# Kernel tuning notes

Measured on AMD Instinct MI355X. Metric: run time of the kernel, lower is better.

The kernel has to match this reference:

```python
import jax, jax.numpy as jnp
import numpy as np

NUM_TREES = 32
TREE_DEPTH = 6
INPUT_DIM = 256
SHRINKAGE = 0.1
PHI_NUMEL = 1
N_INTERNAL = (1 << TREE_DEPTH) - 1  # 63, heap-ordered (level by level)
N_LEAVES = 1 << TREE_DEPTH          # 64


def setup_inputs() -> dict:
    key = jax.random.key(0)
    kx, kw, kb, kp = jax.random.split(key, 4)
    x = jax.random.normal(kx, (16384, INPUT_DIM), dtype=jnp.float32)
    # All internal-node Linear(input_dim,1) weights, batched: [T, N, F], biases [T, N]
    lim = 1.0 / np.sqrt(INPUT_DIM)  # torch nn.Linear default uniform init scale
    W = jax.random.uniform(kw, (NUM_TREES, N_INTERNAL, INPUT_DIM), minval=-lim, maxval=lim, dtype=jnp.float32)
    b = jax.random.uniform(kb, (NUM_TREES, N_INTERNAL), minval=-lim, maxval=lim, dtype=jnp.float32)
    # Leaf values phi: [T, L, P] (original: randn per leaf)
    phi = jax.random.normal(kp, (NUM_TREES, N_LEAVES, PHI_NUMEL), dtype=jnp.float32)
    return {"x": x, "W": W, "b": b, "phi": phi}


def reference(x, W, b, phi):
    B = x.shape[0]
    T, N, F = W.shape
    # One batched GEMM for every internal node of every tree, then sigmoid.
    # probs[b, t, n] = sigmoid(x[b] . W[t, n] + b[t, n]); heap order: node n at
    # level d occupies slots [2^d - 1, 2^(d+1) - 2], children of slot i are 2i, 2i+1.
    probs = jax.nn.sigmoid(jnp.einsum('bf,tnf->btn', x, W) + b)  # [B, T, N]
    # Path probabilities down the tree: left child gets (1 - p), right gets p
    # (matches calculate_probabilities: left <- pp*(1-prob), right <- pp*prob).
    mu = jnp.ones((B, T, 1), dtype=probs.dtype)
    offset = 0
    depth = int(np.log2(N + 1))
    for d in range(depth):
        n = 1 << d
        p = probs[:, :, offset:offset + n]                      # [B, T, n]
        mu = jnp.stack([mu * (1.0 - p), mu * p], axis=-1)       # [B, T, n, 2]
        mu = mu.reshape(B, T, 2 * n)
        offset += n
    # mu: [B, T, L] leaf path probabilities. Per-tree pred = sum_l mu_l * phi_l;
    # GBM output = shrinkage * sum over trees.
    pred = SHRINKAGE * jnp.einsum('btl,tlp->bp', mu, phi)       # [B, P]
    return pred
```

## Files before the change

kernel.cpp:

```cpp
#include <hip/hip_runtime.h>
#include <cmath>

typedef unsigned short u16;
typedef __bf16 bf16x8 __attribute__((ext_vector_type(8)));
typedef float f32x4 __attribute__((ext_vector_type(4)));
typedef unsigned short u16x4 __attribute__((ext_vector_type(4)));

#define BATCH 16384
#define NTREE 32
#define NINT 63
#define NLEAF 64
#define FDIM 256
#define MT 128
#define BK 64
#define KSTEPS 4

typedef __attribute__((address_space(3))) void lvoid;
typedef __attribute__((address_space(1))) const void gvoid;
__device__ __forceinline__ void gload16(const void* g, void* l) {
    __builtin_amdgcn_global_load_lds((gvoid*)g, (lvoid*)l, 16, 0, 0);
}

__device__ __forceinline__ u16 f2bf(float f) {
    unsigned int x = __float_as_uint(f);
    x += 0x7fffu + ((x >> 16) & 1u);
    return (u16)(x >> 16);
}

__global__ void convert_kernel(const float* __restrict__ x, const float* __restrict__ W,
                               u16* __restrict__ xb, u16* __restrict__ Wb) {
    int idx = blockIdx.x * blockDim.x + threadIdx.x;
    int stride = gridDim.x * blockDim.x;
    const int NXQ = BATCH * FDIM / 4;
    for (int i = idx; i < NXQ; i += stride) {
        float4 v = ((const float4*)x)[i];
        u16x4 o = { f2bf(v.x), f2bf(v.y), f2bf(v.z), f2bf(v.w) };
        ((u16x4*)xb)[i] = o;
    }
    const int NWQ = NTREE * NLEAF * FDIM / 4;
    for (int i = idx; i < NWQ; i += stride) {
        int t = i / (NLEAF * FDIM / 4);
        int r = i % (NLEAF * FDIM / 4);
        int node = r / (FDIM / 4);
        int kq = r % (FDIM / 4);
        float4 v = make_float4(0.f, 0.f, 0.f, 0.f);
        if (node < NINT) v = ((const float4*)(W + ((size_t)t * NINT + node) * FDIM))[kq];
        u16x4 o = { f2bf(v.x), f2bf(v.y), f2bf(v.z), f2bf(v.w) };
        ((u16x4*)Wb)[i] = o;
    }
}

__global__ __launch_bounds__(256, 3) void softgbm_main(
    const u16* __restrict__ xb, const u16* __restrict__ Wb,
    const float* __restrict__ bg, const float* __restrict__ phig,
    float* __restrict__ partial) {
    union ShMem {
        struct { u16 A[2][MT * BK]; u16 B[2][NLEAF * BK]; } s;
        struct { float p[MT * 65]; float phi[NLEAF]; } e;
    };
    __shared__ ShMem sh;

    const int tid = threadIdx.x;
    const int lane = tid & 63, wv = tid >> 6;
    const int t = blockIdx.y;
    const int m0 = blockIdx.x * MT;

    const u16* agp[4]; const u16* bgp[2];
    #pragma unroll
    for (int j = 0; j < 4; ++j) {
        int cl = wv * 256 + j * 64 + lane;
        int row = cl >> 3, pcc = cl & 7;
        int cc = pcc ^ (row & 7);
        agp[j] = xb + (size_t)(m0 + row) * FDIM + cc * 8;
    }
    #pragma unroll
    for (int j = 0; j < 2; ++j) {
        int cl = wv * 128 + j * 64 + lane;
        int row = cl >> 3, pcc = cl & 7;
        int cc = pcc ^ (row & 7);
        bgp[j] = Wb + (size_t)(t * NLEAF + row) * FDIM + cc * 8;
    }

    const int wr = wv >> 1, wc = wv & 1;
    const int frow = lane & 15, lg = lane >> 4;
    int aoffs[4][2], boffs[2][2];
    #pragma unroll
    for (int ar = 0; ar < 4; ++ar) {
        int r = wr * 64 + ar * 16 + frow;
        #pragma unroll
        for (int ks = 0; ks < 2; ++ks) {
            int cc = ks * 4 + lg;
            aoffs[ar][ks] = r * 128 + ((cc ^ (r & 7)) * 16);
        }
    }
    #pragma unroll
    for (int bc = 0; bc < 2; ++bc) {
        int n = wc * 32 + bc * 16 + frow;
        #pragma unroll
        for (int ks = 0; ks < 2; ++ks) {
            int cc = ks * 4 + lg;
            boffs[bc][ks] = n * 128 + ((cc ^ (n & 7)) * 16);
        }
    }

    float bv[2];
    #pragma unroll
    for (int bc = 0; bc < 2; ++bc) {
        int col = wc * 32 + bc * 16 + frow;
        bv[bc] = (col < NINT) ? bg[t * NINT + col] : 0.f;
    }

    #pragma unroll
    for (int j = 0; j < 4; ++j)
        gload16(agp[j], &sh.s.A[0][(wv * 256 + j * 64) * 8]);
    #pragma unroll
    for (int j = 0; j < 2; ++j)
        gload16(bgp[j], &sh.s.B[0][(wv * 128 + j * 64) * 8]);
    __syncthreads();

    f32x4 acc[4][2] = {};
    #pragma unroll
    for (int st = 0; st < KSTEPS; ++st) {
        int cur = st & 1;
        if (st < KSTEPS - 1) {
            int nxt = cur ^ 1;
            #pragma unroll
            for (int j = 0; j < 4; ++j)
                gload16(agp[j] + (st + 1) * BK, &sh.s.A[nxt][(wv * 256 + j * 64) * 8]);
            #pragma unroll
            for (int j = 0; j < 2; ++j)
                gload16(bgp[j] + (st + 1) * BK, &sh.s.B[nxt][(wv * 128 + j * 64) * 8]);
        }
        const char* Ab = (const char*)sh.s.A[cur];
        const char* Bb = (const char*)sh.s.B[cur];
        #pragma unroll
        for (int ks = 0; ks < 2; ++ks) {
            bf16x8 af[4], bf_[2];
            #pragma unroll
            for (int ar = 0; ar < 4; ++ar) af[ar] = *(const bf16x8*)(Ab + aoffs[ar][ks]);
            #pragma unroll
            for (int bc = 0; bc < 2; ++bc) bf_[bc] = *(const bf16x8*)(Bb + boffs[bc][ks]);
            #pragma unroll
            for (int ar = 0; ar < 4; ++ar)
                #pragma unroll
                for (int bc = 0; bc < 2; ++bc)
                    acc[ar][bc] = __builtin_amdgcn_mfma_f32_16x16x32_bf16(af[ar], bf_[bc], acc[ar][bc], 0, 0, 0);
        }
        __syncthreads();
    }

    if (tid < NLEAF) sh.e.phi[tid] = phig[(size_t)t * NLEAF + tid];
    #pragma unroll
    for (int ar = 0; ar < 4; ++ar)
        #pragma unroll
        for (int bc = 0; bc < 2; ++bc)
            #pragma unroll
            for (int j = 0; j < 4; ++j) {
                int row = wr * 64 + ar * 16 + lg * 4 + j;
                int col = wc * 32 + bc * 16 + frow;
                float z = acc[ar][bc][j] + bv[bc];
                sh.e.p[row * 65 + col] = __builtin_amdgcn_rcpf(1.f + __expf(-z));
            }
    __syncthreads();

    {
        const int row = tid >> 1, hl = tid & 1;
        const float* pr = sh.e.p + row * 65;
        const float* pf = sh.e.phi + hl * 32;
        float p0 = pr[0];
        float mu[16];
        mu[0] = hl ? p0 : 1.f - p0;
        #pragma unroll
        for (int d = 1; d < 5; ++d) {
            int n = 1 << (d - 1);
            int off = (1 << d) - 1 + hl * n;
            #pragma unroll
            for (int i = n - 1; i >= 0; --i) {
                float p = pr[off + i];
                float m = mu[i];
                float tt = m * p;
                mu[2 * i + 1] = tt;
                mu[2 * i] = m - tt;
            }
        }
        float s = 0.f;
        #pragma unroll
        for (int i = 0; i < 16; ++i) {
            float p = pr[31 + hl * 16 + i];
            float a = pf[2 * i], b2 = pf[2 * i + 1];
            s += mu[i] * (a + p * (b2 - a));
        }
        s += __shfl_xor(s, 1);
        if (!hl) partial[(size_t)t * BATCH + m0 + row] = s;
    }
}

__global__ void reduce_kernel(const float* __restrict__ partial, float* __restrict__ out) {
    int i = blockIdx.x * 256 + threadIdx.x;
    float s = 0.f;
    #pragma unroll
    for (int t = 0; t < NTREE; ++t) s += partial[(size_t)t * BATCH + i];
    out[i] = 0.1f * s;
}

extern "C" void kernel_launch(void* const* d_in, const int* in_sizes, int n_in,
                              void* d_out, int out_size, void* d_ws, size_t ws_size,
                              hipStream_t stream) {
    const float* x   = (const float*)d_in[0];
    const float* W   = (const float*)d_in[1];
    const float* b   = (const float*)d_in[2];
    const float* phi = (const float*)d_in[3];
    float* out = (float*)d_out;

    u16* xb = (u16*)d_ws;
    u16* Wb = xb + (size_t)BATCH * FDIM;
    float* partial = (float*)(Wb + (size_t)NTREE * NLEAF * FDIM);

    convert_kernel<<<2048, 256, 0, stream>>>(x, W, xb, Wb);
    softgbm_main<<<dim3(BATCH / MT, NTREE), 256, 0, stream>>>(xb, Wb, b, phi, partial);
    reduce_kernel<<<BATCH / 256, 256, 0, stream>>>(partial, out);
}
```

Measured before the change: 45.24 us.

## Process two trees per block to reuse the staged x tile

Each block now computes the node GEMM for two trees at once, so the x tile loaded into LDS serves a 128x128 output instead of 128x64. This halves the redundant global and LDS traffic for x across trees and halves the grid. The epilogue is rewritten so each thread walks a full tree for one row rather than splitting the tree across a thread pair with a shuffle. In exchange, accumulator and mu register use rises, the occupancy hint is dropped, LDS grows, and there are fewer blocks.

```diff
diff --git a/kernel.cpp b/kernel.cpp
--- a/kernel.cpp
+++ b/kernel.cpp
@@ -12,6 +12,7 @@
 #define NLEAF 64
 #define FDIM 256
 #define MT 128
+#define TPB 2
 #define BK 64
 #define KSTEPS 4
 
@@ -50,40 +51,35 @@
     }
 }
 
-__global__ __launch_bounds__(256, 3) void softgbm_main(
+__global__ __launch_bounds__(256) void softgbm_main(
     const u16* __restrict__ xb, const u16* __restrict__ Wb,
     const float* __restrict__ bg, const float* __restrict__ phig,
     float* __restrict__ partial) {
     union ShMem {
-        struct { u16 A[2][MT * BK]; u16 B[2][NLEAF * BK]; } s;
-        struct { float p[MT * 65]; float phi[NLEAF]; } e;
+        struct { u16 A[2][MT * BK]; u16 B[2][TPB * NLEAF * BK]; } s;
+        struct { float p[TPB][MT][65]; float phi[TPB][NLEAF]; } e;
     };
     __shared__ ShMem sh;
 
     const int tid = threadIdx.x;
     const int lane = tid & 63, wv = tid >> 6;
-    const int t = blockIdx.y;
+    const int t0 = blockIdx.y * TPB;
     const int m0 = blockIdx.x * MT;
-
-    const u16* agp[4]; const u16* bgp[2];
+    const int bw0 = blockIdx.y * TPB * NLEAF;
+
+    const u16* agp[4]; const u16* bgp[4];
     #pragma unroll
     for (int j = 0; j < 4; ++j) {
         int cl = wv * 256 + j * 64 + lane;
         int row = cl >> 3, pcc = cl & 7;
         int cc = pcc ^ (row & 7);
         agp[j] = xb + (size_t)(m0 + row) * FDIM + cc * 8;
-    }
-    #pragma unroll
-    for (int j = 0; j < 2; ++j) {
-        int cl = wv * 128 + j * 64 + lane;
-        int row = cl >> 3, pcc = cl & 7;
-        int cc = pcc ^ (row & 7);
-        bgp[j] = Wb + (size_t)(t * NLEAF + row) * FDIM + cc * 8;
+        bgp[j] = Wb + (size_t)(bw0 + row) * FDIM + cc * 8;
     }
 
     const int wr = wv >> 1, wc = wv & 1;
     const int frow = lane & 15, lg = lane >> 4;
-    int aoffs[4][2], boffs[2][2];
+    int aoffs[4][2], boffs[4][2];
     #pragma unroll
     for (int ar = 0; ar < 4; ++ar) {
         int r = wr * 64 + ar * 16 + frow;
@@ -94,8 +90,8 @@
         }
     }
     #pragma unroll
-    for (int bc = 0; bc < 2; ++bc) {
-        int n = wc * 32 + bc * 16 + frow;
+    for (int bc = 0; bc < 4; ++bc) {
+        int n = wc * 64 + bc * 16 + frow;
         #pragma unroll
         for (int ks = 0; ks < 2; ++ks) {
             int cc = ks * 4 + lg;
@@ -103,77 +99,76 @@
         }
     }
 
-    float bv[2];
-    #pragma unroll
-    for (int bc = 0; bc < 2; ++bc) {
-        int col = wc * 32 + bc * 16 + frow;
-        bv[bc] = (col < NINT) ? bg[t * NINT + col] : 0.f;
-    }
-
-    #pragma unroll
-    for (int j = 0; j < 4; ++j)
+    float bv[4];
+    #pragma unroll
+    for (int bc = 0; bc < 4; ++bc) {
+        int col = bc * 16 + frow;
+        bv[bc] = (col < NINT) ? bg[(t0 + wc) * NINT + col] : 0.f;
+    }
+    if (tid < TPB * NLEAF)
+        sh.e.phi[tid >> 6][tid & 63] = phig[(size_t)(t0 + (tid >> 6)) * NLEAF + (tid & 63)];
+
+    #pragma unroll
+    for (int j = 0; j < 4; ++j) {
         gload16(agp[j], &sh.s.A[0][(wv * 256 + j * 64) * 8]);
-    #pragma unroll
-    for (int j = 0; j < 2; ++j)
-        gload16(bgp[j], &sh.s.B[0][(wv * 128 + j * 64) * 8]);
+        gload16(bgp[j], &sh.s.B[0][(wv * 256 + j * 64) * 8]);
+    }
     __syncthreads();
 
-    f32x4 acc[4][2] = {};
+    f32x4 acc[4][4] = {};
     #pragma unroll
     for (int st = 0; st < KSTEPS; ++st) {
         int cur = st & 1;
         if (st < KSTEPS - 1) {
             int nxt = cur ^ 1;
             #pragma unroll
-            for (int j = 0; j < 4; ++j)
+            for (int j = 0; j < 4; ++j) {
                 gload16(agp[j] + (st + 1) * BK, &sh.s.A[nxt][(wv * 256 + j * 64) * 8]);
-            #pragma unroll
-            for (int j = 0; j < 2; ++j)
-                gload16(bgp[j] + (st + 1) * BK, &sh.s.B[nxt][(wv * 128 + j * 64) * 8]);
+                gload16(bgp[j] + (st + 1) * BK, &sh.s.B[nxt][(wv * 256 + j * 64) * 8]);
+            }
         }
         const char* Ab = (const char*)sh.s.A[cur];
         const char* Bb = (const char*)sh.s.B[cur];
         #pragma unroll
         for (int ks = 0; ks < 2; ++ks) {
-            bf16x8 af[4], bf_[2];
+            bf16x8 af[4], bf_[4];
             #pragma unroll
             for (int ar = 0; ar < 4; ++ar) af[ar] = *(const bf16x8*)(Ab + aoffs[ar][ks]);
             #pragma unroll
-            for (int bc = 0; bc < 2; ++bc) bf_[bc] = *(const bf16x8*)(Bb + boffs[bc][ks]);
+            for (int bc = 0; bc < 4; ++bc) bf_[bc] = *(const bf16x8*)(Bb + boffs[bc][ks]);
             #pragma unroll
             for (int ar = 0; ar < 4; ++ar)
                 #pragma unroll
-                for (int bc = 0; bc < 2; ++bc)
+                for (int bc = 0; bc < 4; ++bc)
                     acc[ar][bc] = __builtin_amdgcn_mfma_f32_16x16x32_bf16(af[ar], bf_[bc], acc[ar][bc], 0, 0, 0);
         }
         __syncthreads();
     }
 
-    if (tid < NLEAF) sh.e.phi[tid] = phig[(size_t)t * NLEAF + tid];
     #pragma unroll
     for (int ar = 0; ar < 4; ++ar)
         #pragma unroll
-        for (int bc = 0; bc < 2; ++bc)
+        for (int bc = 0; bc < 4; ++bc)
             #pragma unroll
             for (int j = 0; j < 4; ++j) {
                 int row = wr * 64 + ar * 16 + lg * 4 + j;
-                int col = wc * 32 + bc * 16 + frow;
+                int col = bc * 16 + frow;
                 float z = acc[ar][bc][j] + bv[bc];
-                sh.e.p[row * 65 + col] = __builtin_amdgcn_rcpf(1.f + __expf(-z));
+                sh.e.p[wc][row][col] = __builtin_amdgcn_rcpf(1.f + __expf(-z));
             }
     __syncthreads();
 
     {
-        const int row = tid >> 1, hl = tid & 1;
-        const float* pr = sh.e.p + row * 65;
-        const float* pf = sh.e.phi + hl * 32;
+        const int th = tid >> 7, row = tid & (MT - 1);
+        const float* pr = &sh.e.p[th][row][0];
+        const float* pf = sh.e.phi[th];
+        float mu[32];
         float p0 = pr[0];
-        float mu[16];
-        mu[0] = hl ? p0 : 1.f - p0;
+        mu[0] = 1.f - p0; mu[1] = p0;
         #pragma unroll
         for (int d = 1; d < 5; ++d) {
-            int n = 1 << (d - 1);
-            int off = (1 << d) - 1 + hl * n;
+            int n = 1 << d;
+            int off = n - 1;
             #pragma unroll
             for (int i = n - 1; i >= 0; --i) {
                 float p = pr[off + i];
@@ -185,13 +180,12 @@
         }
         float s = 0.f;
         #pragma unroll
-        for (int i = 0; i < 16; ++i) {
-            float p = pr[31 + hl * 16 + i];
+        for (int i = 0; i < 32; ++i) {
+            float p = pr[31 + i];
             float a = pf[2 * i], b2 = pf[2 * i + 1];
             s += mu[i] * (a + p * (b2 - a));
         }
-        s += __shfl_xor(s, 1);
-        if (!hl) partial[(size_t)t * BATCH + m0 + row] = s;
+        partial[(size_t)(t0 + th) * BATCH + m0 + row] = s;
     }
 }
 
@@ -217,6 +211,6 @@
     float* partial = (float*)(Wb + (size_t)NTREE * NLEAF * FDIM);
 
     convert_kernel<<<2048, 256, 0, stream>>>(x, W, xb, Wb);
-    softgbm_main<<<dim3(BATCH / MT, NTREE), 256, 0, stream>>>(xb, Wb, b, phi, partial);
+    softgbm_main<<<dim3(BATCH / MT, NTREE / TPB), 256, 0, stream>>>(xb, Wb, b, phi, partial);
     reduce_kernel<<<BATCH / 256, 256, 0, stream>>>(partial, out);
 }
```

Result: faster. 43.06 us (-4.8%).
